# Performance work log

Hardware: AMD Instinct MI355X
Metric: run time of the kernel (lower is better)

Reference implementation:

```python
import jax, jax.numpy as jnp
import numpy as np

N_OSC = 50
N_PER = 40
DT = 0.01
STEPS = 100
# one-link torque limb physical constants (reconstructed)
M_G_LC = 1.0   # m*g*lc gravity torque coefficient
B_DAMP = 0.1   # viscous damping
I_INERTIA = 1.0


def setup_inputs() -> dict:
    key = jax.random.key(0)
    ks = jax.random.split(key, 16)
    B = 8192
    x = jax.random.normal(ks[0], (B, 2), dtype=jnp.float32)
    fc1_w = jax.random.normal(ks[1], (128, 2), dtype=jnp.float32) * 0.5
    fc1_b = jax.random.normal(ks[2], (128,), dtype=jnp.float32) * 0.1
    fc2_w = jax.random.normal(ks[3], (128, 128), dtype=jnp.float32) * 0.08
    fc2_b = jax.random.normal(ks[4], (128,), dtype=jnp.float32) * 0.1
    fc3_w = jax.random.normal(ks[5], (N_OSC * 2, 128), dtype=jnp.float32) * 0.08
    fc3_b = jax.random.normal(ks[6], (N_OSC * 2,), dtype=jnp.float32) * 0.1
    fcd_w = jax.random.normal(ks[7], (1, 128), dtype=jnp.float32) * 0.001  # weight/100
    fcd_b = jnp.zeros((1,), dtype=jnp.float32)                            # bias*0
    enc = jax.random.normal(ks[8], (N_OSC, N_PER, 2), dtype=jnp.float32)
    obias = jax.random.normal(ks[9], (N_OSC, N_PER), dtype=jnp.float32)
    dec = jax.random.normal(ks[10], (N_OSC, 2, N_PER), dtype=jnp.float32) * 0.05
    fc4_w = jax.random.normal(ks[11], (1, N_OSC * N_PER), dtype=jnp.float32) * 1e-4  # weight/10000
    fc4_b = jnp.zeros((1,), dtype=jnp.float32)                                       # bias*0
    return {"x": x, "fc1_w": fc1_w, "fc1_b": fc1_b, "fc2_w": fc2_w, "fc2_b": fc2_b,
            "fc3_w": fc3_w, "fc3_b": fc3_b, "fcd_w": fcd_w, "fcd_b": fcd_b,
            "enc": enc, "obias": obias, "dec": dec, "fc4_w": fc4_w, "fc4_b": fc4_b}


def reference(x, fc1_w, fc1_b, fc2_w, fc2_b, fc3_w, fc3_b, fcd_w, fcd_b,
              enc, obias, dec, fc4_w, fc4_b):
    B = x.shape[0]
    h = jax.nn.relu(x @ fc1_w.T + fc1_b)            # (B,128)
    direct = h @ fcd_w.T + fcd_b                    # (B,1)
    h2 = jax.nn.relu(h @ fc2_w.T + fc2_b)           # (B,128)
    x3 = h2 @ fc3_w.T + fc3_b                       # (B, 2*N_OSC)
    o0 = x3.reshape(B, N_OSC, 2).transpose(1, 0, 2)  # (N_OSC,B,2), xi = x[:, 2j:2j+2]
    l0 = jnp.concatenate([x[:, :1], jnp.zeros((B, 1), dtype=x.dtype)], axis=1)  # (B,2)

    def step(carry, _):
        o, l = carry
        # NEF oscillator activities: relu(state @ encoders^T + bias), vectorized over oscillators
        a = jax.nn.relu(jnp.einsum('obd,ond->obn', o, enc) + obias[:, None, :])  # (N_OSC,B,N_PER)
        o_deriv = jnp.einsum('odn,obn->obd', dec, a)                             # (N_OSC,B,2)
        o = o + DT * o_deriv
        acts = a.transpose(1, 0, 2).reshape(B, N_OSC * N_PER)                    # (B,2000)
        torque = (acts @ fc4_w.T + fc4_b + direct)[:, 0]                         # (B,)
        theta, omega = l[:, 0], l[:, 1]
        alpha = (torque - M_G_LC * jnp.sin(theta) - B_DAMP * omega) / I_INERTIA
        l = l + DT * jnp.stack([omega, alpha], axis=1)
        return (o, l), (l, torque)

    _, (l_states, torques) = jax.lax.scan(step, (o0, l0), None, length=STEPS)
    return l_states, torques  # (STEPS,B,2), (STEPS,B)
```

## Files before the change

### kernel.cpp

```cpp
#include <hip/hip_runtime.h>

#define N_OSC 50
#define N_PER 40
#define DT 0.01f
#define STEPS 100
#define BATCH 8192

typedef float v2f __attribute__((ext_vector_type(2)));

static __device__ __forceinline__ v2f fma2(v2f a, v2f b, v2f c) {
    return __builtin_elementwise_fma(a, b, c);
}

#define WS_PC     0
#define WS_DIRECT 12288
#define WS_O0     20480
#define WS_TORQ   839680

__global__ void pack_consts(const float* __restrict__ enc,
                            const float* __restrict__ obias,
                            const float* __restrict__ dec,
                            const float* __restrict__ fc4_w,
                            float* __restrict__ pc) {
    int idx = blockIdx.x * blockDim.x + threadIdx.x;
    if (idx >= N_OSC * N_PER) return;
    int o = idx / N_PER, n = idx % N_PER;
    int i = n >> 1, h = n & 1;
    float* base = pc + o * 240;
    base[4 * i + h]           = enc[o * 80 + 2 * n + 0];
    base[4 * i + 2 + h]       = enc[o * 80 + 2 * n + 1];
    base[80 + 4 * i + h]      = dec[o * 80 + n];
    base[80 + 4 * i + 2 + h]  = dec[o * 80 + 40 + n];
    base[160 + 2 * i + h]     = fc4_w[o * 40 + n];
    base[200 + n]             = obias[o * 40 + n];
}

__global__ __launch_bounds__(256) void torq_zero(float* __restrict__ torq) {
    int i = blockIdx.x * 256 + threadIdx.x;
    ((float4*)torq)[i] = make_float4(0.f, 0.f, 0.f, 0.f);
}

__global__ __launch_bounds__(512) void mlp_kernel(
    const float* __restrict__ x,
    const float* __restrict__ fc1_w, const float* __restrict__ fc1_b,
    const float* __restrict__ fc2_w, const float* __restrict__ fc2_b,
    const float* __restrict__ fc3_w, const float* __restrict__ fc3_b,
    const float* __restrict__ fcd_w, const float* __restrict__ fcd_b,
    float* __restrict__ o0out, float* __restrict__ directout) {
    __shared__ float hs[64 * 132];
    __shared__ float h2s[64 * 132];
    int tid = threadIdx.x;
    int lane = tid & 63;
    int wv = __builtin_amdgcn_readfirstlane(tid >> 6);
    int b0 = blockIdx.x * 64;

    for (int idx = tid; idx < 64 * 128; idx += 512) {
        int bb = idx >> 7, j = idx & 127;
        float x0 = x[(b0 + bb) * 2], x1 = x[(b0 + bb) * 2 + 1];
        float v = fmaf(x0, fc1_w[j * 2], fmaf(x1, fc1_w[j * 2 + 1], fc1_b[j]));
        hs[bb * 132 + j] = fmaxf(v, 0.f);
    }
    __syncthreads();

    if (tid < 64) {
        float s = fcd_b[0];
        #pragma unroll 8
        for (int k = 0; k < 128; k += 4) {
            float4 h4 = *(const float4*)&hs[tid * 132 + k];
            float4 w4 = *(const float4*)&fcd_w[k];
            s = fmaf(h4.x, w4.x, fmaf(h4.y, w4.y, fmaf(h4.z, w4.z, fmaf(h4.w, w4.w, s))));
        }
        directout[b0 + tid] = s;
    }

    for (int pass = 0; pass < 4; ++pass) {
        int j0 = wv * 16 + pass * 4;
        float a0 = fc2_b[j0], a1 = fc2_b[j0 + 1], a2 = fc2_b[j0 + 2], a3 = fc2_b[j0 + 3];
        const float* w0 = fc2_w + j0 * 128;
        const float* w1 = w0 + 128;
        const float* w2 = w0 + 256;
        const float* w3 = w0 + 384;
        #pragma unroll 8
        for (int k = 0; k < 128; k += 4) {
            float4 h4 = *(const float4*)&hs[lane * 132 + k];
            float4 q0 = *(const float4*)&w0[k];
            float4 q1 = *(const float4*)&w1[k];
            float4 q2 = *(const float4*)&w2[k];
            float4 q3 = *(const float4*)&w3[k];
            a0 = fmaf(h4.x, q0.x, fmaf(h4.y, q0.y, fmaf(h4.z, q0.z, fmaf(h4.w, q0.w, a0))));
            a1 = fmaf(h4.x, q1.x, fmaf(h4.y, q1.y, fmaf(h4.z, q1.z, fmaf(h4.w, q1.w, a1))));
            a2 = fmaf(h4.x, q2.x, fmaf(h4.y, q2.y, fmaf(h4.z, q2.z, fmaf(h4.w, q2.w, a2))));
            a3 = fmaf(h4.x, q3.x, fmaf(h4.y, q3.y, fmaf(h4.z, q3.z, fmaf(h4.w, q3.w, a3))));
        }
        h2s[lane * 132 + j0]     = fmaxf(a0, 0.f);
        h2s[lane * 132 + j0 + 1] = fmaxf(a1, 0.f);
        h2s[lane * 132 + j0 + 2] = fmaxf(a2, 0.f);
        h2s[lane * 132 + j0 + 3] = fmaxf(a3, 0.f);
    }
    __syncthreads();

    for (int pass = 0; pass < 4; ++pass) {
        int j0 = pass * 32 + wv * 4;
        if (j0 >= 100) continue;
        float a0 = fc3_b[j0], a1 = fc3_b[j0 + 1], a2 = fc3_b[j0 + 2], a3 = fc3_b[j0 + 3];
        const float* w0 = fc3_w + j0 * 128;
        const float* w1 = w0 + 128;
        const float* w2 = w0 + 256;
        const float* w3 = w0 + 384;
        #pragma unroll 8
        for (int k = 0; k < 128; k += 4) {
            float4 h4 = *(const float4*)&h2s[lane * 132 + k];
            float4 q0 = *(const float4*)&w0[k];
            float4 q1 = *(const float4*)&w1[k];
            float4 q2 = *(const float4*)&w2[k];
            float4 q3 = *(const float4*)&w3[k];
            a0 = fmaf(h4.x, q0.x, fmaf(h4.y, q0.y, fmaf(h4.z, q0.z, fmaf(h4.w, q0.w, a0))));
            a1 = fmaf(h4.x, q1.x, fmaf(h4.y, q1.y, fmaf(h4.z, q1.z, fmaf(h4.w, q1.w, a1))));
            a2 = fmaf(h4.x, q2.x, fmaf(h4.y, q2.y, fmaf(h4.z, q2.z, fmaf(h4.w, q2.w, a2))));
            a3 = fmaf(h4.x, q3.x, fmaf(h4.y, q3.y, fmaf(h4.z, q3.z, fmaf(h4.w, q3.w, a3))));
        }
        o0out[(j0)     * BATCH + b0 + lane] = a0;
        o0out[(j0 + 1) * BATCH + b0 + lane] = a1;
        o0out[(j0 + 2) * BATCH + b0 + lane] = a2;
        o0out[(j0 + 3) * BATCH + b0 + lane] = a3;
    }
}

__global__ __launch_bounds__(64, 2) void osc_kernel(const float* __restrict__ pc,
                                                    const float* __restrict__ o0init,
                                                    float* __restrict__ torq) {
    __shared__ float cs[240];
    int blk = blockIdx.x;
    int bg = blk / N_OSC;
    int osc = blk - bg * N_OSC;
    int tid = threadIdx.x;
    int b = bg * 64 + tid;

    if (tid < 60)
        ((float4*)cs)[tid] = ((const float4*)(pc + osc * 240))[tid];
    __syncthreads();

    v2f e0[20], e1[20], d0c[20], d1c[20], wc[20];
    #pragma unroll
    for (int i = 0; i < 20; ++i) {
        e0[i]  = *(const v2f*)(cs + 4 * i);
        e1[i]  = *(const v2f*)(cs + 4 * i + 2);
        d0c[i] = *(const v2f*)(cs + 80 + 4 * i);
        d1c[i] = *(const v2f*)(cs + 80 + 4 * i + 2);
    }
    #pragma unroll
    for (int i = 0; i < 20; ++i) wc[i] = *(const v2f*)(cs + 160 + 2 * i);

    float ob[40];
    #pragma unroll
    for (int n = 0; n < 40; ++n) {
        union { float f; int i; } u;
        u.f = cs[200 + n];
        u.i = __builtin_amdgcn_readfirstlane(u.i);
        ob[n] = u.f;
    }

    float s0 = o0init[(2 * osc) * BATCH + b];
    float s1 = o0init[(2 * osc + 1) * BATCH + b];

    for (int step = 0; step < STEPS; ++step) {
        v2f o0p = (v2f){s0, s0};
        v2f o1p = (v2f){s1, s1};
        v2f tq = (v2f){0.f, 0.f};
        v2f D0 = (v2f){0.f, 0.f};
        v2f D1 = (v2f){0.f, 0.f};
        #pragma unroll
        for (int i = 0; i < 20; ++i) {
            v2f obp = (v2f){ob[2 * i], ob[2 * i + 1]};
            v2f a = fma2(o0p, e0[i], fma2(o1p, e1[i], obp));
            a = __builtin_elementwise_max(a, (v2f){0.f, 0.f});
            tq = fma2(a, wc[i], tq);
            D0 = fma2(a, d0c[i], D0);
            D1 = fma2(a, d1c[i], D1);
        }
        s0 = fmaf(DT, D0.x + D0.y, s0);
        s1 = fmaf(DT, D1.x + D1.y, s1);
        atomicAdd(&torq[step * BATCH + b], tq.x + tq.y);
    }
}

__global__ __launch_bounds__(64) void pend_kernel(const float* __restrict__ x,
                                                  const float* __restrict__ torq,
                                                  const float* __restrict__ direct,
                                                  const float* __restrict__ fc4_b,
                                                  float* __restrict__ out) {
    int b = blockIdx.x * 64 + threadIdx.x;
    float theta = x[2 * b];
    float omega = 0.f;
    float base = direct[b] + fc4_b[0];
    float2* out_l = (float2*)out;
    float* out_t = out + STEPS * BATCH * 2;
    float pf[4];
    #pragma unroll
    for (int j = 0; j < 4; ++j) pf[j] = torq[j * BATCH + b];
    #pragma unroll 4
    for (int s = 0; s < STEPS; ++s) {
        float tq = base + pf[s & 3];
        if (s + 4 < STEPS) pf[s & 3] = torq[(s + 4) * BATCH + b];
        float alpha = tq - __sinf(theta) - 0.1f * omega;
        theta = fmaf(DT, omega, theta);
        omega = fmaf(DT, alpha, omega);
        out_l[s * BATCH + b] = make_float2(theta, omega);
        out_t[s * BATCH + b] = tq;
    }
}

extern "C" void kernel_launch(void* const* d_in, const int* in_sizes, int n_in,
                              void* d_out, int out_size, void* d_ws, size_t ws_size,
                              hipStream_t stream) {
    const float* x     = (const float*)d_in[0];
    const float* fc1_w = (const float*)d_in[1];
    const float* fc1_b = (const float*)d_in[2];
    const float* fc2_w = (const float*)d_in[3];
    const float* fc2_b = (const float*)d_in[4];
    const float* fc3_w = (const float*)d_in[5];
    const float* fc3_b = (const float*)d_in[6];
    const float* fcd_w = (const float*)d_in[7];
    const float* fcd_b = (const float*)d_in[8];
    const float* enc   = (const float*)d_in[9];
    const float* obias = (const float*)d_in[10];
    const float* dec   = (const float*)d_in[11];
    const float* fc4_w = (const float*)d_in[12];
    const float* fc4_b = (const float*)d_in[13];
    float* out = (float*)d_out;
    float* ws = (float*)d_ws;

    float* pc      = ws + WS_PC;
    float* direct  = ws + WS_DIRECT;
    float* o0      = ws + WS_O0;
    float* torq    = ws + WS_TORQ;

    hipLaunchKernelGGL(pack_consts, dim3(8), dim3(256), 0, stream,
                       enc, obias, dec, fc4_w, pc);
    hipLaunchKernelGGL(torq_zero, dim3(STEPS * BATCH / 4 / 256), dim3(256), 0, stream,
                       torq);
    hipLaunchKernelGGL(mlp_kernel, dim3(128), dim3(512), 0, stream,
                       x, fc1_w, fc1_b, fc2_w, fc2_b, fc3_w, fc3_b,
                       fcd_w, fcd_b, o0, direct);
    hipLaunchKernelGGL(osc_kernel, dim3(128 * N_OSC), dim3(64), 0, stream,
                       pc, o0, torq);
    hipLaunchKernelGGL(pend_kernel, dim3(BATCH / 64), dim3(64), 0, stream,
                       x, torq, direct, fc4_b, out);
}
```

Baseline: 429.0 us.

## Fuse prep kernels, shrink MLP blocks, pin osc constants, widen pend blocks

Merges the constant-packing and torque-zeroing kernels into one launch, which removes one kernel launch. The MLP now handles 32 batch rows per 256-thread block, giving 256 blocks so more CUs have work, though the weight reads are amortized over fewer rows. Empty asm barriers force the oscillator constants to stay in VGPRs so the compiler cannot rematerialize them. The pendulum kernel moves to 256-thread blocks.

New measurement: 414.2 us. -3.4%, faster.

```diff
diff --git a/kernel.cpp b/kernel.cpp
--- a/kernel.cpp
+++ b/kernel.cpp
@@ -17,52 +17,48 @@
 #define WS_O0     20480
 #define WS_TORQ   839680
 
-__global__ void pack_consts(const float* __restrict__ enc,
-                            const float* __restrict__ obias,
-                            const float* __restrict__ dec,
-                            const float* __restrict__ fc4_w,
-                            float* __restrict__ pc) {
-    int idx = blockIdx.x * blockDim.x + threadIdx.x;
-    if (idx >= N_OSC * N_PER) return;
-    int o = idx / N_PER, n = idx % N_PER;
-    int i = n >> 1, h = n & 1;
-    float* base = pc + o * 240;
-    base[4 * i + h]           = enc[o * 80 + 2 * n + 0];
-    base[4 * i + 2 + h]       = enc[o * 80 + 2 * n + 1];
-    base[80 + 4 * i + h]      = dec[o * 80 + n];
-    base[80 + 4 * i + 2 + h]  = dec[o * 80 + 40 + n];
-    base[160 + 2 * i + h]     = fc4_w[o * 40 + n];
-    base[200 + n]             = obias[o * 40 + n];
-}
-
-__global__ __launch_bounds__(256) void torq_zero(float* __restrict__ torq) {
-    int i = blockIdx.x * 256 + threadIdx.x;
-    ((float4*)torq)[i] = make_float4(0.f, 0.f, 0.f, 0.f);
-}
-
-__global__ __launch_bounds__(512) void mlp_kernel(
+__global__ __launch_bounds__(256) void prep_kernel(
+    const float* __restrict__ enc, const float* __restrict__ obias,
+    const float* __restrict__ dec, const float* __restrict__ fc4_w,
+    float* __restrict__ pc, float* __restrict__ torq) {
+    int idx = blockIdx.x * 256 + threadIdx.x;
+    ((float4*)torq)[idx] = make_float4(0.f, 0.f, 0.f, 0.f);
+    if (idx < N_OSC * N_PER) {
+        int o = idx / N_PER, n = idx - o * N_PER;
+        int i = n >> 1, h = n & 1;
+        float* base = pc + o * 240;
+        base[4 * i + h]           = enc[o * 80 + 2 * n + 0];
+        base[4 * i + 2 + h]       = enc[o * 80 + 2 * n + 1];
+        base[80 + 4 * i + h]      = dec[o * 80 + n];
+        base[80 + 4 * i + 2 + h]  = dec[o * 80 + 40 + n];
+        base[160 + 2 * i + h]     = fc4_w[o * 40 + n];
+        base[200 + n]             = obias[o * 40 + n];
+    }
+}
+
+__global__ __launch_bounds__(256) void mlp_kernel(
     const float* __restrict__ x,
     const float* __restrict__ fc1_w, const float* __restrict__ fc1_b,
     const float* __restrict__ fc2_w, const float* __restrict__ fc2_b,
     const float* __restrict__ fc3_w, const float* __restrict__ fc3_b,
     const float* __restrict__ fcd_w, const float* __restrict__ fcd_b,
     float* __restrict__ o0out, float* __restrict__ directout) {
-    __shared__ float hs[64 * 132];
-    __shared__ float h2s[64 * 132];
+    __shared__ float hs[32 * 132];
+    __shared__ float h2s[32 * 132];
     int tid = threadIdx.x;
-    int lane = tid & 63;
-    int wv = __builtin_amdgcn_readfirstlane(tid >> 6);
-    int b0 = blockIdx.x * 64;
-
-    for (int idx = tid; idx < 64 * 128; idx += 512) {
-        int bb = idx >> 7, j = idx & 127;
-        float x0 = x[(b0 + bb) * 2], x1 = x[(b0 + bb) * 2 + 1];
+    int bb = tid & 31;
+    int hw = tid >> 5;
+    int b0 = blockIdx.x * 32;
+
+    for (int idx = tid; idx < 32 * 128; idx += 256) {
+        int r = idx >> 7, j = idx & 127;
+        float x0 = x[(b0 + r) * 2], x1 = x[(b0 + r) * 2 + 1];
         float v = fmaf(x0, fc1_w[j * 2], fmaf(x1, fc1_w[j * 2 + 1], fc1_b[j]));
-        hs[bb * 132 + j] = fmaxf(v, 0.f);
+        hs[r * 132 + j] = fmaxf(v, 0.f);
     }
     __syncthreads();
 
-    if (tid < 64) {
+    if (tid < 32) {
         float s = fcd_b[0];
         #pragma unroll 8
         for (int k = 0; k < 128; k += 4) {
@@ -74,7 +70,7 @@
     }
 
     for (int pass = 0; pass < 4; ++pass) {
-        int j0 = wv * 16 + pass * 4;
+        int j0 = hw * 16 + pass * 4;
         float a0 = fc2_b[j0], a1 = fc2_b[j0 + 1], a2 = fc2_b[j0 + 2], a3 = fc2_b[j0 + 3];
         const float* w0 = fc2_w + j0 * 128;
         const float* w1 = w0 + 128;
@@ -82,7 +78,7 @@
         const float* w3 = w0 + 384;
         #pragma unroll 8
         for (int k = 0; k < 128; k += 4) {
-            float4 h4 = *(const float4*)&hs[lane * 132 + k];
+            float4 h4 = *(const float4*)&hs[bb * 132 + k];
             float4 q0 = *(const float4*)&w0[k];
             float4 q1 = *(const float4*)&w1[k];
             float4 q2 = *(const float4*)&w2[k];
@@ -92,15 +88,15 @@
             a2 = fmaf(h4.x, q2.x, fmaf(h4.y, q2.y, fmaf(h4.z, q2.z, fmaf(h4.w, q2.w, a2))));
             a3 = fmaf(h4.x, q3.x, fmaf(h4.y, q3.y, fmaf(h4.z, q3.z, fmaf(h4.w, q3.w, a3))));
         }
-        h2s[lane * 132 + j0]     = fmaxf(a0, 0.f);
-        h2s[lane * 132 + j0 + 1] = fmaxf(a1, 0.f);
-        h2s[lane * 132 + j0 + 2] = fmaxf(a2, 0.f);
-        h2s[lane * 132 + j0 + 3] = fmaxf(a3, 0.f);
+        h2s[bb * 132 + j0]     = fmaxf(a0, 0.f);
+        h2s[bb * 132 + j0 + 1] = fmaxf(a1, 0.f);
+        h2s[bb * 132 + j0 + 2] = fmaxf(a2, 0.f);
+        h2s[bb * 132 + j0 + 3] = fmaxf(a3, 0.f);
     }
     __syncthreads();
 
     for (int pass = 0; pass < 4; ++pass) {
-        int j0 = pass * 32 + wv * 4;
+        int j0 = pass * 32 + hw * 4;
         if (j0 >= 100) continue;
         float a0 = fc3_b[j0], a1 = fc3_b[j0 + 1], a2 = fc3_b[j0 + 2], a3 = fc3_b[j0 + 3];
         const float* w0 = fc3_w + j0 * 128;
@@ -109,7 +105,7 @@
         const float* w3 = w0 + 384;
         #pragma unroll 8
         for (int k = 0; k < 128; k += 4) {
-            float4 h4 = *(const float4*)&h2s[lane * 132 + k];
+            float4 h4 = *(const float4*)&h2s[bb * 132 + k];
             float4 q0 = *(const float4*)&w0[k];
             float4 q1 = *(const float4*)&w1[k];
             float4 q2 = *(const float4*)&w2[k];
@@ -119,10 +115,10 @@
             a2 = fmaf(h4.x, q2.x, fmaf(h4.y, q2.y, fmaf(h4.z, q2.z, fmaf(h4.w, q2.w, a2))));
             a3 = fmaf(h4.x, q3.x, fmaf(h4.y, q3.y, fmaf(h4.z, q3.z, fmaf(h4.w, q3.w, a3))));
         }
-        o0out[(j0)     * BATCH + b0 + lane] = a0;
-        o0out[(j0 + 1) * BATCH + b0 + lane] = a1;
-        o0out[(j0 + 2) * BATCH + b0 + lane] = a2;
-        o0out[(j0 + 3) * BATCH + b0 + lane] = a3;
+        o0out[(j0)     * BATCH + b0 + bb] = a0;
+        o0out[(j0 + 1) * BATCH + b0 + bb] = a1;
+        o0out[(j0 + 2) * BATCH + b0 + bb] = a2;
+        o0out[(j0 + 3) * BATCH + b0 + bb] = a3;
     }
 }
 
@@ -147,9 +143,16 @@
         e1[i]  = *(const v2f*)(cs + 4 * i + 2);
         d0c[i] = *(const v2f*)(cs + 80 + 4 * i);
         d1c[i] = *(const v2f*)(cs + 80 + 4 * i + 2);
-    }
-    #pragma unroll
-    for (int i = 0; i < 20; ++i) wc[i] = *(const v2f*)(cs + 160 + 2 * i);
+        wc[i]  = *(const v2f*)(cs + 160 + 2 * i);
+    }
+    #pragma unroll
+    for (int i = 0; i < 20; ++i) {
+        asm volatile("" : "+v"(e0[i]));
+        asm volatile("" : "+v"(e1[i]));
+        asm volatile("" : "+v"(d0c[i]));
+        asm volatile("" : "+v"(d1c[i]));
+        asm volatile("" : "+v"(wc[i]));
+    }
 
     float ob[40];
     #pragma unroll
@@ -184,12 +187,12 @@
     }
 }
 
-__global__ __launch_bounds__(64) void pend_kernel(const float* __restrict__ x,
-                                                  const float* __restrict__ torq,
-                                                  const float* __restrict__ direct,
-                                                  const float* __restrict__ fc4_b,
-                                                  float* __restrict__ out) {
-    int b = blockIdx.x * 64 + threadIdx.x;
+__global__ __launch_bounds__(256) void pend_kernel(const float* __restrict__ x,
+                                                   const float* __restrict__ torq,
+                                                   const float* __restrict__ direct,
+                                                   const float* __restrict__ fc4_b,
+                                                   float* __restrict__ out) {
+    int b = blockIdx.x * 256 + threadIdx.x;
     float theta = x[2 * b];
     float omega = 0.f;
     float base = direct[b] + fc4_b[0];
@@ -235,15 +238,13 @@
     float* o0      = ws + WS_O0;
     float* torq    = ws + WS_TORQ;
 
-    hipLaunchKernelGGL(pack_consts, dim3(8), dim3(256), 0, stream,
-                       enc, obias, dec, fc4_w, pc);
-    hipLaunchKernelGGL(torq_zero, dim3(STEPS * BATCH / 4 / 256), dim3(256), 0, stream,
-                       torq);
-    hipLaunchKernelGGL(mlp_kernel, dim3(128), dim3(512), 0, stream,
+    hipLaunchKernelGGL(prep_kernel, dim3(STEPS * BATCH / 4 / 256), dim3(256), 0, stream,
+                       enc, obias, dec, fc4_w, pc, torq);
+    hipLaunchKernelGGL(mlp_kernel, dim3(256), dim3(256), 0, stream,
                        x, fc1_w, fc1_b, fc2_w, fc2_b, fc3_w, fc3_b,
                        fcd_w, fcd_b, o0, direct);
     hipLaunchKernelGGL(osc_kernel, dim3(128 * N_OSC), dim3(64), 0, stream,
                        pc, o0, torq);
-    hipLaunchKernelGGL(pend_kernel, dim3(BATCH / 64), dim3(64), 0, stream,
+    hipLaunchKernelGGL(pend_kernel, dim3(BATCH / 256), dim3(256), 0, stream,
                        x, torq, direct, fc4_b, out);
 }
```
